# Performance work log

Measured on AMD Instinct MI355X. Metric: run time of the kernel, lower is better.

Reference implementation:

```python
import jax, jax.numpy as jnp
import numpy as np

D = 4096  # in_features == rotation_size (power of 2 -> K == 1, no extra hadamard_K matmul)


def matmul_hadU(x):
    """Normalized Walsh-Hadamard transform along the last axis, matching the
    torch recursive-butterfly matmul_hadU (K == 1 branch)."""
    n = x.shape[-1]
    shape = x.shape
    v = x.reshape(-1, n, 1)  # (B*, m, c) with m*c == n
    while v.shape[1] > 1:
        b_, m, c = v.shape
        v = v.reshape(b_, m // 2, 2, c)
        a, b = v[:, :, 0, :], v[:, :, 1, :]
        # view(b_, m//2, 2*c): [a+b | a-b] along the channel axis
        v = jnp.concatenate([a + b, a - b], axis=-1)
    return v.reshape(shape) / jnp.sqrt(jnp.asarray(n, x.dtype))


def setup_inputs() -> dict:
    key = jax.random.key(0)
    k_x, k_w, k_b = jax.random.split(key, 3)
    x = jax.random.normal(k_x, (4, 2048, D), dtype=jnp.float32)
    W = jax.random.normal(k_w, (D, D), dtype=jnp.float32) * 0.02  # nn.Linear weight [out, in]
    b = jax.random.normal(k_b, (D,), dtype=jnp.float32) * 0.02
    return {"x": x, "W": W, "b": b}


def reference(x, W, b):
    x_rot = matmul_hadU(x)                 # [B, S, D]
    return jnp.einsum('bsd,od->bso', x_rot, W) + b
```

## Files before the change

### kernel.cpp

```cpp
#include <hip/hip_runtime.h>
#include <hip/hip_bf16.h>


#define D_DIM 4096
#define M_ROWS 8192

typedef float f32x4 __attribute__((ext_vector_type(4)));
typedef __bf16 bf16x8 __attribute__((ext_vector_type(8)));

__device__ __forceinline__ unsigned short f2bf(float f) {
  unsigned int u = __float_as_uint(f);
  return (unsigned short)((u + 0x7fffu + ((u >> 16) & 1u)) >> 16);
}

__device__ __forceinline__ void async16(const void* g, void* l) {
  __builtin_amdgcn_global_load_lds(
      (const __attribute__((address_space(1))) unsigned int*)g,
      (__attribute__((address_space(3))) unsigned int*)l, 16, 0, 0);
}

#define WHT_AS 280
#define WHT_BS 17

__global__ __launch_bounds__(256) void wht_cast_rows(
    const float* __restrict__ X, unsigned short* __restrict__ Y) {
  __shared__ float s[16 * WHT_AS];
  const int row = blockIdx.x;
  const float* xr = X + (size_t)row * D_DIM;
  const int t = threadIdx.x;
  float v[16];

#pragma unroll
  for (int a = 0; a < 16; ++a) v[a] = xr[a * 256 + t];
#pragma unroll
  for (int h = 1; h < 16; h <<= 1) {
#pragma unroll
    for (int i = 0; i < 16; ++i) {
      if ((i & h) == 0) {
        float p = v[i], q = v[i + h];
        v[i] = p + q;
        v[i + h] = p - q;
      }
    }
  }
  {
    const int base = (t >> 4) * WHT_BS + (t & 15);
#pragma unroll
    for (int a = 0; a < 16; ++a) s[a * WHT_AS + base] = v[a];
  }
  __syncthreads();

  {
    const int base = (t >> 4) * WHT_AS + (t & 15);
#pragma unroll
    for (int b = 0; b < 16; ++b) v[b] = s[base + b * WHT_BS];
#pragma unroll
    for (int h = 1; h < 16; h <<= 1) {
#pragma unroll
      for (int i = 0; i < 16; ++i) {
        if ((i & h) == 0) {
          float p = v[i], q = v[i + h];
          v[i] = p + q;
          v[i + h] = p - q;
        }
      }
    }
#pragma unroll
    for (int b = 0; b < 16; ++b) s[base + b * WHT_BS] = v[b];
  }
  __syncthreads();

  {
    const int base = (t >> 4) * WHT_AS + (t & 15) * WHT_BS;
#pragma unroll
    for (int c = 0; c < 16; ++c) v[c] = s[base + c];
#pragma unroll
    for (int h = 1; h < 16; h <<= 1) {
#pragma unroll
      for (int i = 0; i < 16; ++i) {
        if ((i & h) == 0) {
          float p = v[i], q = v[i + h];
          v[i] = p + q;
          v[i + h] = p - q;
        }
      }
    }
    union {
      unsigned short us[16];
      uint4 q4[2];
    } pk;
#pragma unroll
    for (int c = 0; c < 16; ++c) pk.us[c] = f2bf(v[c] * 0.015625f);
    uint4* dst =
        (uint4*)(Y + (size_t)row * D_DIM + (t >> 4) * 256 + (t & 15) * 16);
    dst[0] = pk.q4[0];
    dst[1] = pk.q4[1];
  }
}

__global__ __launch_bounds__(256) void cast_w(const float* __restrict__ W,
                                              unsigned short* __restrict__ Wb) {
  const size_t i = ((size_t)blockIdx.x * 256 + threadIdx.x) * 8;
  const float4* p = (const float4*)(W + i);
  float4 f0 = p[0], f1 = p[1];
  union {
    unsigned short us[8];
    uint4 q;
  } pk;
  pk.us[0] = f2bf(f0.x);
  pk.us[1] = f2bf(f0.y);
  pk.us[2] = f2bf(f0.z);
  pk.us[3] = f2bf(f0.w);
  pk.us[4] = f2bf(f1.x);
  pk.us[5] = f2bf(f1.y);
  pk.us[6] = f2bf(f1.z);
  pk.us[7] = f2bf(f1.w);
  *(uint4*)(Wb + i) = pk.q;
}

#define GNT 64

__global__ __launch_bounds__(512, 2) void gemm256_bias(
    const unsigned short* __restrict__ A,
    const unsigned short* __restrict__ B,
    const float* __restrict__ bias, float* __restrict__ C) {
  constexpr int K = 4096, N = 4096;
  __shared__ unsigned short sm[65536];

  const int tid = threadIdx.x;
  const int l = tid & 63;
  const int w = tid >> 6;
  const int wm = w >> 2;
  const int wn = w & 3;
  const int row16 = l & 15;
  const int kgrp = l >> 4;

  const int orig = blockIdx.x;
  const int wgid = (orig & 7) * 64 + (orig >> 3);
  const int bn = wgid & 15;
  const int bm = wgid >> 4;
  const int m0 = bm * 256, n0 = bn * 256;

  const int srcRow = (w >> 1) * 16 + (l >> 2);
  const int srcCol = (w & 1) * 32 + ((((l & 3) << 4) ^ ((l >> 5) << 5)) >> 1);
  const unsigned short* aS = A + (size_t)(m0 + srcRow) * K + srcCol;
  const unsigned short* bS = B + (size_t)(n0 + srcRow) * K + srcCol;
  const int dstBase = tid * 8;

#define STG_A(b, h, kt)                                                       \
  do {                                                                        \
    async16(aS + (size_t)((h)*128) * K + (kt)*64,                             \
            &sm[(b)*32768 + (h)*8192 + dstBase]);                             \
    async16(aS + (size_t)((h)*128 + 64) * K + (kt)*64,                        \
            &sm[(b)*32768 + (h)*8192 + 4096 + dstBase]);                      \
  } while (0)
#define STG_B(b, h, kt)                                                       \
  do {                                                                        \
    async16(bS + (size_t)((h)*128) * K + (kt)*64,                             \
            &sm[(b)*32768 + 16384 + (h)*8192 + dstBase]);                     \
    async16(bS + (size_t)((h)*128 + 64) * K + (kt)*64,                        \
            &sm[(b)*32768 + 16384 + (h)*8192 + 4096 + dstBase]);              \
  } while (0)

  const int laneRd = row16 * 32 + ((kgrp << 3) ^ ((row16 >> 3) << 4));

  f32x4 acc[8][4];
#pragma unroll
  for (int i = 0; i < 8; ++i)
#pragma unroll
    for (int j = 0; j < 4; ++j) acc[i][j] = (f32x4){0.f, 0.f, 0.f, 0.f};

  STG_A(0, 0, 0);
  STG_A(0, 1, 0);
  STG_B(0, 0, 0);
  STG_B(0, 1, 0);
  STG_A(1, 0, 1);
  STG_A(1, 1, 1);
  STG_B(1, 0, 1);
  asm volatile("s_waitcnt vmcnt(6)" ::: "memory");
  __builtin_amdgcn_s_barrier();

#define MFMA1(mf, nf, ks)                                             \
  acc[mf][nf] = __builtin_amdgcn_mfma_f32_16x16x32_bf16(              \
      af[mf][ks], bfm[nf][ks], acc[mf][nf], 0, 0, 0)
#define MFMA_GROUP(g)                                                 \
  MFMA1(2 * g + 0, 0, 0);                                             \
  MFMA1(2 * g + 0, 1, 0);                                             \
  MFMA1(2 * g + 0, 2, 0);                                             \
  MFMA1(2 * g + 0, 3, 0);                                             \
  MFMA1(2 * g + 1, 0, 0);                                             \
  MFMA1(2 * g + 1, 1, 0);                                             \
  MFMA1(2 * g + 1, 2, 0);                                             \
  MFMA1(2 * g + 1, 3, 0);                                             \
  MFMA1(2 * g + 0, 0, 1);                                             \
  MFMA1(2 * g + 0, 1, 1);                                             \
  MFMA1(2 * g + 0, 2, 1);                                             \
  MFMA1(2 * g + 0, 3, 1);                                             \
  MFMA1(2 * g + 1, 0, 1);                                             \
  MFMA1(2 * g + 1, 1, 1);                                             \
  MFMA1(2 * g + 1, 2, 1);                                             \
  MFMA1(2 * g + 1, 3, 1);

  int cur = 0;
  for (int T = 0; T < GNT; ++T) {
    const int base = cur * 32768;
    const unsigned short* pA = &sm[base + wm * 8192 + laneRd];
    const unsigned short* pB =
        &sm[base + 16384 + (wn >> 1) * 8192 + (wn & 1) * 4096 + laneRd];

    bf16x8 af[8][2], bfm[4][2];
#pragma unroll
    for (int mf = 0; mf < 8; ++mf) {
      af[mf][0] = *(const bf16x8*)&pA[mf * 1024];
      af[mf][1] = *(const bf16x8*)&pA[mf * 1024 + 512];
    }
#pragma unroll
    for (int nf = 0; nf < 4; ++nf) {
      bfm[nf][0] = *(const bf16x8*)&pB[nf * 1024];
      bfm[nf][1] = *(const bf16x8*)&pB[nf * 1024 + 512];
    }
    if (T + 1 < GNT) STG_B(cur ^ 1, 1, T + 1);
    __builtin_amdgcn_s_barrier();
    asm volatile("s_waitcnt lgkmcnt(0)" ::: "memory");
    __builtin_amdgcn_s_setprio(1);
    MFMA_GROUP(0);
    __builtin_amdgcn_s_setprio(0);
    __builtin_amdgcn_s_barrier();

    if (T + 2 < GNT) STG_A(cur, 0, T + 2);
    __builtin_amdgcn_s_barrier();
    __builtin_amdgcn_s_setprio(1);
    MFMA_GROUP(1);
    __builtin_amdgcn_s_setprio(0);
    __builtin_amdgcn_s_barrier();

    if (T + 2 < GNT) STG_A(cur, 1, T + 2);
    __builtin_amdgcn_s_barrier();
    __builtin_amdgcn_s_setprio(1);
    MFMA_GROUP(2);
    __builtin_amdgcn_s_setprio(0);
    __builtin_amdgcn_s_barrier();

    if (T + 2 < GNT) STG_B(cur, 0, T + 2);
    __builtin_amdgcn_s_barrier();
    __builtin_amdgcn_s_setprio(1);
    MFMA_GROUP(3);
    __builtin_amdgcn_s_setprio(0);
    if (T < GNT - 2)
      asm volatile("s_waitcnt vmcnt(6)" ::: "memory");
    else
      asm volatile("s_waitcnt vmcnt(0)" ::: "memory");
    __builtin_amdgcn_s_barrier();
    cur ^= 1;
  }

  const int mb = m0 + wm * 128 + kgrp * 4;
  const int nb = n0 + wn * 64 + row16;
  float bv[4];
#pragma unroll
  for (int nf = 0; nf < 4; ++nf) bv[nf] = bias[nb + nf * 16];
#pragma unroll
  for (int mf = 0; mf < 8; ++mf)
#pragma unroll
    for (int nf = 0; nf < 4; ++nf)
#pragma unroll
      for (int r = 0; r < 4; ++r)
        C[(size_t)(mb + mf * 16 + r) * N + nb + nf * 16] =
            acc[mf][nf][r] + bv[nf];
}

extern "C" void kernel_launch(void* const* d_in, const int* in_sizes, int n_in,
                              void* d_out, int out_size, void* d_ws,
                              size_t ws_size, hipStream_t stream) {
  const float* x = (const float*)d_in[0];
  const float* W = (const float*)d_in[1];
  const float* b = (const float*)d_in[2];
  float* out = (float*)d_out;

  unsigned short* Xr = (unsigned short*)d_ws;
  unsigned short* Wb = Xr + (size_t)M_ROWS * D_DIM;

  wht_cast_rows<<<M_ROWS, 256, 0, stream>>>(x, Xr);
  cast_w<<<(D_DIM * (size_t)D_DIM / 8) / 256, 256, 0, stream>>>(W, Wb);
  gemm256_bias<<<512, 512, 0, stream>>>(Xr, Wb, b, out);
}
```

Baseline: 496.9 us.

## Split LDS fragment reads into two phases and reschedule B tile prefetch

The GEMM main loop now loads only half of the A and B fragments from LDS before the first MFMA quadrant and loads the other half while that quadrant computes. The MFMA work is regrouped into 2D quadrants (4 m-fragments by 2 n-fragments) instead of row pairs. Both B-half prefetches for the next tile are issued inside the same iteration rather than one tile ahead, and the vmcnt waits are adjusted to match. The aim is to overlap LDS reads with MFMA and to rebalance global-load issue, at the cost of a shorter prefetch distance for B and more barriers.

```diff
diff --git a/kernel.cpp b/kernel.cpp
--- a/kernel.cpp
+++ b/kernel.cpp
@@ -176,30 +176,16 @@
   STG_B(0, 1, 0);
   STG_A(1, 0, 1);
   STG_A(1, 1, 1);
-  STG_B(1, 0, 1);
-  asm volatile("s_waitcnt vmcnt(6)" ::: "memory");
+  asm volatile("s_waitcnt vmcnt(4)" ::: "memory");
   __builtin_amdgcn_s_barrier();
 
-#define MFMA1(mf, nf, ks)                                             \
-  acc[mf][nf] = __builtin_amdgcn_mfma_f32_16x16x32_bf16(              \
-      af[mf][ks], bfm[nf][ks], acc[mf][nf], 0, 0, 0)
-#define MFMA_GROUP(g)                                                 \
-  MFMA1(2 * g + 0, 0, 0);                                             \
-  MFMA1(2 * g + 0, 1, 0);                                             \
-  MFMA1(2 * g + 0, 2, 0);                                             \
-  MFMA1(2 * g + 0, 3, 0);                                             \
-  MFMA1(2 * g + 1, 0, 0);                                             \
-  MFMA1(2 * g + 1, 1, 0);                                             \
-  MFMA1(2 * g + 1, 2, 0);                                             \
-  MFMA1(2 * g + 1, 3, 0);                                             \
-  MFMA1(2 * g + 0, 0, 1);                                             \
-  MFMA1(2 * g + 0, 1, 1);                                             \
-  MFMA1(2 * g + 0, 2, 1);                                             \
-  MFMA1(2 * g + 0, 3, 1);                                             \
-  MFMA1(2 * g + 1, 0, 1);                                             \
-  MFMA1(2 * g + 1, 1, 1);                                             \
-  MFMA1(2 * g + 1, 2, 1);                                             \
-  MFMA1(2 * g + 1, 3, 1);
+#define MFMA_G(MB, NB)                                                       \
+  _Pragma("unroll") for (int ks = 0; ks < 2; ++ks)                           \
+      _Pragma("unroll") for (int mf = 0; mf < 4; ++mf)                       \
+          _Pragma("unroll") for (int nf = 0; nf < 2; ++nf) acc[MB + mf]      \
+              [NB + nf] = __builtin_amdgcn_mfma_f32_16x16x32_bf16(           \
+                  af[MB + mf][ks], bfm[NB + nf][ks], acc[MB + mf][NB + nf],  \
+                  0, 0, 0);
 
   int cur = 0;
   for (int T = 0; T < GNT; ++T) {
@@ -207,47 +193,60 @@
     const unsigned short* pA = &sm[base + wm * 8192 + laneRd];
     const unsigned short* pB =
         &sm[base + 16384 + (wn >> 1) * 8192 + (wn & 1) * 4096 + laneRd];
-
     bf16x8 af[8][2], bfm[4][2];
-#pragma unroll
-    for (int mf = 0; mf < 8; ++mf) {
+
+#pragma unroll
+    for (int mf = 0; mf < 4; ++mf) {
       af[mf][0] = *(const bf16x8*)&pA[mf * 1024];
       af[mf][1] = *(const bf16x8*)&pA[mf * 1024 + 512];
     }
 #pragma unroll
-    for (int nf = 0; nf < 4; ++nf) {
+    for (int nf = 0; nf < 2; ++nf) {
       bfm[nf][0] = *(const bf16x8*)&pB[nf * 1024];
       bfm[nf][1] = *(const bf16x8*)&pB[nf * 1024 + 512];
     }
+    if (T + 1 < GNT) STG_B(cur ^ 1, 0, T + 1);
+    asm volatile("s_waitcnt lgkmcnt(8)" ::: "memory");
+    __builtin_amdgcn_s_barrier();
+    asm volatile("s_waitcnt lgkmcnt(0)" ::: "memory");
+    __builtin_amdgcn_s_setprio(1);
+    MFMA_G(0, 0);
+    __builtin_amdgcn_s_setprio(0);
+    __builtin_amdgcn_s_barrier();
+
+#pragma unroll
+    for (int mf = 4; mf < 8; ++mf) {
+      af[mf][0] = *(const bf16x8*)&pA[mf * 1024];
+      af[mf][1] = *(const bf16x8*)&pA[mf * 1024 + 512];
+    }
+#pragma unroll
+    for (int nf = 2; nf < 4; ++nf) {
+      bfm[nf][0] = *(const bf16x8*)&pB[nf * 1024];
+      bfm[nf][1] = *(const bf16x8*)&pB[nf * 1024 + 512];
+    }
     if (T + 1 < GNT) STG_B(cur ^ 1, 1, T + 1);
+    asm volatile("s_waitcnt lgkmcnt(8)" ::: "memory");
     __builtin_amdgcn_s_barrier();
     asm volatile("s_waitcnt lgkmcnt(0)" ::: "memory");
     __builtin_amdgcn_s_setprio(1);
-    MFMA_GROUP(0);
+    MFMA_G(4, 0);
     __builtin_amdgcn_s_setprio(0);
     __builtin_amdgcn_s_barrier();
 
     if (T + 2 < GNT) STG_A(cur, 0, T + 2);
     __builtin_amdgcn_s_barrier();
     __builtin_amdgcn_s_setprio(1);
-    MFMA_GROUP(1);
+    MFMA_G(0, 2);
     __builtin_amdgcn_s_setprio(0);
     __builtin_amdgcn_s_barrier();
 
     if (T + 2 < GNT) STG_A(cur, 1, T + 2);
     __builtin_amdgcn_s_barrier();
     __builtin_amdgcn_s_setprio(1);
-    MFMA_GROUP(2);
-    __builtin_amdgcn_s_setprio(0);
-    __builtin_amdgcn_s_barrier();
-
-    if (T + 2 < GNT) STG_B(cur, 0, T + 2);
-    __builtin_amdgcn_s_barrier();
-    __builtin_amdgcn_s_setprio(1);
-    MFMA_GROUP(3);
+    MFMA_G(4, 2);
     __builtin_amdgcn_s_setprio(0);
     if (T < GNT - 2)
-      asm volatile("s_waitcnt vmcnt(6)" ::: "memory");
+      asm volatile("s_waitcnt vmcnt(4)" ::: "memory");
     else
       asm volatile("s_waitcnt vmcnt(0)" ::: "memory");
     __builtin_amdgcn_s_barrier();
```

New measurement: 486.4 us. 2.1% less time.
